# Optimization experiments

Hardware: AMD Instinct MI355X
Metric: run time of the kernel (lower is better)

Reference implementation:

```python
import jax, jax.numpy as jnp
import numpy as np

B, IN, H, E, N_EP, V_DIM = 4096, 1024, 16, 256, 2048, 64


def setup_inputs() -> dict:
    key = jax.random.key(0)
    k_x, k_c, k_w, k_k, k_v = jax.random.split(key, 5)
    x = jax.random.normal(k_x, (B, IN), dtype=jnp.float32)
    curiosity_score = jax.random.normal(k_c, (B,), dtype=jnp.float32)
    # toqueries: Linear(IN, E*H, bias=False); store as [IN, E*H] for x @ Wq
    Wq = jax.random.normal(k_w, (IN, E * H), dtype=jnp.float32) * (1.0 / np.sqrt(IN))
    # offline_keys [n_episodes, emb_size]; buffer repeats over heads (identical), so keep 2D
    keys = jax.random.normal(k_k, (N_EP, E), dtype=jnp.float32)
    # values buffer = offline_values.abs().mean(dim=-1) -> [n_episodes]
    offline_values = jax.random.normal(k_v, (N_EP, V_DIM), dtype=jnp.float32)
    values = jnp.abs(offline_values).mean(axis=-1)
    return {"x": x, "curiosity_score": curiosity_score, "Wq": Wq, "keys": keys, "values": values}


def reference(x, curiosity_score, Wq, keys, values):
    b = x.shape[0]
    # queries: [b, h, e], scaled by e**(1/4) (keys left unscaled, as in source)
    q = (x @ Wq).reshape(b, H, E) / (E ** 0.25)
    # dot: [b, h, n_episodes]; keys identical across heads -> single contraction
    dot = jnp.einsum("bhe,ne->bhn", q, keys) + values[None, None, :]
    dot = jax.nn.softmax(dot, axis=-1)
    # curiosity reweighting: scale probabilities then re-softmax (not scale-invariant)
    cur = jnp.exp(curiosity_score).reshape(b, 1, 1)
    dot = jax.nn.softmax(dot * cur, axis=-1)
    # head-mean -> [b, n_episodes]
    return dot.mean(axis=1)
```

## Files before the change

kernel.cpp:

```cpp
#include <hip/hip_runtime.h>


typedef __attribute__((ext_vector_type(8))) short bf16x8;
typedef __attribute__((ext_vector_type(4))) float f32x4;

typedef const __attribute__((address_space(1))) void* gcptr;
typedef __attribute__((address_space(3))) void* sptr;

__device__ __forceinline__ void gload16(const void* g, void* l) {
  __builtin_amdgcn_global_load_lds((gcptr)g, (sptr)l, 16, 0, 0);
}

__device__ __forceinline__ unsigned short f2bf(float f) {
  unsigned int u = __float_as_uint(f);
  unsigned int r = (u + 0x7fffu + ((u >> 16) & 1u)) >> 16;
  return (unsigned short)r;
}
__device__ __forceinline__ float bf2f(unsigned short s) {
  return __uint_as_float(((unsigned int)s) << 16);
}

__global__ void k_split(const float* __restrict__ src,
                        unsigned short* __restrict__ hi,
                        unsigned short* __restrict__ lo, int n4) {
  int i = blockIdx.x * blockDim.x + threadIdx.x;
  if (i >= n4) return;
  float4 v = reinterpret_cast<const float4*>(src)[i];
  ushort4 h, l;
  h.x = f2bf(v.x); l.x = f2bf(v.x - bf2f(h.x));
  h.y = f2bf(v.y); l.y = f2bf(v.y - bf2f(h.y));
  h.z = f2bf(v.z); l.z = f2bf(v.z - bf2f(h.z));
  h.w = f2bf(v.w); l.w = f2bf(v.w - bf2f(h.w));
  reinterpret_cast<ushort4*>(hi)[i] = h;
  reinterpret_cast<ushort4*>(lo)[i] = l;
}

__global__ void k_prepk(const float* __restrict__ keys,
                        unsigned short* __restrict__ th,
                        unsigned short* __restrict__ tl) {
  int g = blockIdx.x * blockDim.x + threadIdx.x;
  int k0 = g >> 13, rem = g & 8191;
  int jg = rem >> 6, lam = rem & 63;
  int row = jg * 16 + (lam & 15);
  int col = k0 * 32 + (lam >> 4) * 8;
  const float* s = keys + (size_t)row * 256 + col;
  float4 v0 = *reinterpret_cast<const float4*>(s);
  float4 v1 = *reinterpret_cast<const float4*>(s + 4);
  ushort4 h0, h1, l0, l1;
  h0.x = f2bf(v0.x); l0.x = f2bf(v0.x - bf2f(h0.x));
  h0.y = f2bf(v0.y); l0.y = f2bf(v0.y - bf2f(h0.y));
  h0.z = f2bf(v0.z); l0.z = f2bf(v0.z - bf2f(h0.z));
  h0.w = f2bf(v0.w); l0.w = f2bf(v0.w - bf2f(h0.w));
  h1.x = f2bf(v1.x); l1.x = f2bf(v1.x - bf2f(h1.x));
  h1.y = f2bf(v1.y); l1.y = f2bf(v1.y - bf2f(h1.y));
  h1.z = f2bf(v1.z); l1.z = f2bf(v1.z - bf2f(h1.z));
  h1.w = f2bf(v1.w); l1.w = f2bf(v1.w - bf2f(h1.w));
  reinterpret_cast<ushort4*>(th + (size_t)g * 8)[0] = h0;
  reinterpret_cast<ushort4*>(th + (size_t)g * 8)[1] = h1;
  reinterpret_cast<ushort4*>(tl + (size_t)g * 8)[0] = l0;
  reinterpret_cast<ushort4*>(tl + (size_t)g * 8)[1] = l1;
}

__global__ void k_twq(const float* __restrict__ W,
                      unsigned short* __restrict__ th,
                      unsigned short* __restrict__ tl) {
  __shared__ float t[64][65];
  int tx = threadIdx.x & 63, ty = threadIdx.x >> 6;
  int c0 = blockIdx.x * 64, r0 = blockIdx.y * 64;
#pragma unroll
  for (int i = 0; i < 64; i += 4)
    t[ty + i][tx] = W[(size_t)(r0 + ty + i) * 4096 + (c0 + tx)] * 0.25f;
  __syncthreads();
#pragma unroll
  for (int i = 0; i < 64; i += 4) {
    float v = t[tx][ty + i];
    unsigned short h = f2bf(v);
    unsigned short l = f2bf(v - bf2f(h));
    size_t o = (size_t)(c0 + ty + i) * 1024 + (r0 + tx);
    th[o] = h; tl[o] = l;
  }
}

__global__ __launch_bounds__(256) void k_gemm1(
    const unsigned short* __restrict__ Ah, const unsigned short* __restrict__ Al,
    const unsigned short* __restrict__ Bh, const unsigned short* __restrict__ Bl,
    unsigned short* __restrict__ Qh, unsigned short* __restrict__ Ql) {
  __shared__ unsigned short As[2][128][32];
  __shared__ unsigned short Bs[2][128][32];
  const int tid = threadIdx.x;
  const int w = tid >> 6, l = tid & 63;
  const int lr = l & 15, lg = l >> 4;
  const int m0 = blockIdx.y * 128, n0 = blockIdx.x * 128;
  const int wr = (w >> 1) * 64, wc = (w & 1) * 64;
  const int srow = tid >> 2;
  const int skel = (tid & 3) * 8;
  f32x4 acc[4][4] = {};

  const size_t gaBase = (size_t)(m0 + srow) * 1024 + skel;
  const size_t gbBase = (size_t)(n0 + srow) * 1024 + skel;
  char* lA0 = (char*)&As[0][0][0] + w * 1024;
  char* lA1 = (char*)&As[1][0][0] + w * 1024;
  char* lB0 = (char*)&Bs[0][0][0] + w * 1024;
  char* lB1 = (char*)&Bs[1][0][0] + w * 1024;

  for (int k0 = 0; k0 < 1024; k0 += 32) {
    gload16(Ah + gaBase + k0,             lA0);
    gload16(Ah + gaBase + 64 * 1024 + k0, lA0 + 4096);
    gload16(Al + gaBase + k0,             lA1);
    gload16(Al + gaBase + 64 * 1024 + k0, lA1 + 4096);
    gload16(Bh + gbBase + k0,             lB0);
    gload16(Bh + gbBase + 64 * 1024 + k0, lB0 + 4096);
    gload16(Bl + gbBase + k0,             lB1);
    gload16(Bl + gbBase + 64 * 1024 + k0, lB1 + 4096);
    __syncthreads();
    bf16x8 ah[4], am[4], bh[4], bm[4];
#pragma unroll
    for (int i = 0; i < 4; ++i) {
      ah[i] = *reinterpret_cast<const bf16x8*>(&As[0][wr + i * 16 + lr][lg * 8]);
      am[i] = *reinterpret_cast<const bf16x8*>(&As[1][wr + i * 16 + lr][lg * 8]);
      bh[i] = *reinterpret_cast<const bf16x8*>(&Bs[0][wc + i * 16 + lr][lg * 8]);
      bm[i] = *reinterpret_cast<const bf16x8*>(&Bs[1][wc + i * 16 + lr][lg * 8]);
    }
#pragma unroll
    for (int i = 0; i < 4; ++i)
#pragma unroll
      for (int j = 0; j < 4; ++j) {
        acc[i][j] = __builtin_amdgcn_mfma_f32_16x16x32_bf16(ah[i], bh[j], acc[i][j], 0, 0, 0);
        acc[i][j] = __builtin_amdgcn_mfma_f32_16x16x32_bf16(am[i], bh[j], acc[i][j], 0, 0, 0);
        acc[i][j] = __builtin_amdgcn_mfma_f32_16x16x32_bf16(ah[i], bm[j], acc[i][j], 0, 0, 0);
      }
    __syncthreads();
  }
#pragma unroll
  for (int i = 0; i < 4; ++i)
#pragma unroll
    for (int j = 0; j < 4; ++j)
#pragma unroll
      for (int r = 0; r < 4; ++r) {
        int row = m0 + wr + i * 16 + lg * 4 + r;
        int col = n0 + wc + j * 16 + lr;
        float v = acc[i][j][r];
        unsigned short hh = f2bf(v);
        unsigned short ll = f2bf(v - bf2f(hh));
        size_t o = (size_t)row * 4096 + col;
        Qh[o] = hh; Ql[o] = ll;
      }
}

#define MFMA_BF16(a, b, c) __builtin_amdgcn_mfma_f32_16x16x32_bf16(a, b, c, 0, 0, 0)

#define C_OF(T) ((unsigned)((((T) >> 4) * 128 + ((T) & 15)) * 1024))

#define LOADB(SLOT, T)                                                        \
  B##SLOT = *reinterpret_cast<const bf16x8*>(kHb + (vbase + C_OF(T)));        \
  L##SLOT = *reinterpret_cast<const bf16x8*>(kLb + (vbase + C_OF(T)));

#define DJST(J0, J1, S0, S1, PF, T0, T1)              \
  __builtin_amdgcn_s_setprio(1);                      \
  acc[0][J0] = MFMA_BF16(ah0, B##S0, acc[0][J0]);     \
  acc[1][J0] = MFMA_BF16(ah1, B##S0, acc[1][J0]);     \
  acc[0][J1] = MFMA_BF16(ah0, B##S1, acc[0][J1]);     \
  acc[1][J1] = MFMA_BF16(ah1, B##S1, acc[1][J1]);     \
  acc[0][J0] = MFMA_BF16(am0, B##S0, acc[0][J0]);     \
  acc[1][J0] = MFMA_BF16(am1, B##S0, acc[1][J0]);     \
  acc[0][J1] = MFMA_BF16(am0, B##S1, acc[0][J1]);     \
  acc[1][J1] = MFMA_BF16(am1, B##S1, acc[1][J1]);     \
  acc[0][J0] = MFMA_BF16(ah0, L##S0, acc[0][J0]);     \
  acc[1][J0] = MFMA_BF16(ah1, L##S0, acc[1][J0]);     \
  acc[0][J1] = MFMA_BF16(ah0, L##S1, acc[0][J1]);     \
  acc[1][J1] = MFMA_BF16(ah1, L##S1, acc[1][J1]);     \
  __builtin_amdgcn_s_setprio(0);                      \
  if (PF) { LOADB(S0, T0) LOADB(S1, T1) }

#define BODY_HEAD(K)                                                   \
  ah0 = *reinterpret_cast<const bf16x8*>(As + ((K)) * 512 + l8);       \
  ah1 = *reinterpret_cast<const bf16x8*>(As + (8 + (K)) * 512 + l8);   \
  am0 = *reinterpret_cast<const bf16x8*>(As + (16 + (K)) * 512 + l8);  \
  am1 = *reinterpret_cast<const bf16x8*>(As + (24 + (K)) * 512 + l8);

#define BODY(K)                                            \
  BODY_HEAD(K)                                             \
  DJST(0,  1,  0, 1, 1, (K) * 16 + 4,  (K) * 16 + 5)       \
  DJST(2,  3,  2, 3, 1, (K) * 16 + 6,  (K) * 16 + 7)       \
  DJST(4,  5,  0, 1, 1, (K) * 16 + 8,  (K) * 16 + 9)       \
  DJST(6,  7,  2, 3, 1, (K) * 16 + 10, (K) * 16 + 11)      \
  DJST(8,  9,  0, 1, 1, (K) * 16 + 12, (K) * 16 + 13)      \
  DJST(10, 11, 2, 3, 1, (K) * 16 + 14, (K) * 16 + 15)      \
  DJST(12, 13, 0, 1, 1, (K) * 16 + 16, (K) * 16 + 17)      \
  DJST(14, 15, 2, 3, 1, (K) * 16 + 18, (K) * 16 + 19)

#define BODY7                              \
  BODY_HEAD(7)                             \
  DJST(0,  1,  0, 1, 1, 116, 117)          \
  DJST(2,  3,  2, 3, 1, 118, 119)          \
  DJST(4,  5,  0, 1, 1, 120, 121)          \
  DJST(6,  7,  2, 3, 1, 122, 123)          \
  DJST(8,  9,  0, 1, 1, 124, 125)          \
  DJST(10, 11, 2, 3, 1, 126, 127)          \
  DJST(12, 13, 0, 1, 0, 0, 0)              \
  DJST(14, 15, 2, 3, 0, 0, 0)

__global__ __launch_bounds__(512, 2) void k_attn(
    const unsigned short* __restrict__ Qh, const unsigned short* __restrict__ Ql,
    const unsigned short* __restrict__ KtH, const unsigned short* __restrict__ KtL,
    const float* __restrict__ values, const float* __restrict__ cur,
    float* __restrict__ out) {
  __shared__ unsigned short As[32 * 512];
  __shared__ float red[8][32];
  const int tid = threadIdx.x;
  const int w = tid >> 6, l = tid & 63;
  const int lr = l & 15, lg = l >> 4;
  const int r0 = blockIdx.x * 32;
  const int cs = (int)((w + blockIdx.x) & 7);
  const int n0 = cs * 256;
  const int l8 = l * 8;

#pragma unroll
  for (int qq = 0; qq < 4; ++qq) {
    const int s = w * 4 + qq;
    const int plane = s >> 4, mf = (s >> 3) & 1, k0s = s & 7;
    const unsigned short* src = plane ? Ql : Qh;
    const size_t ga = (size_t)(r0 + mf * 16 + lr) * 256 + k0s * 32 + lg * 8;
    gload16(src + ga, (char*)As + s * 1024);
  }
  __syncthreads();

  const unsigned sliceB = (unsigned)__builtin_amdgcn_readfirstlane(cs * 16384);
  const char* kHb = (const char*)KtH + sliceB;
  const char* kLb = (const char*)KtL + sliceB;
  const unsigned vbase = (unsigned)(l * 16);

  f32x4 acc[2][16] = {};
  bf16x8 B0, B1, B2, B3, L0, L1, L2, L3;
  bf16x8 ah0, ah1, am0, am1;

  LOADB(0, 0) LOADB(1, 1) LOADB(2, 2) LOADB(3, 3)

  BODY(0) BODY(1) BODY(2) BODY(3) BODY(4) BODY(5) BODY(6) BODY7

#pragma unroll
  for (int j = 0; j < 16; ++j) {
    float vv = values[n0 + j * 16 + lr];
#pragma unroll
    for (int mf = 0; mf < 2; ++mf)
#pragma unroll
      for (int r = 0; r < 4; ++r) acc[mf][j][r] += vv;
  }

  const int rb = lg * 4;
  float M1[2][4];
#pragma unroll
  for (int mf = 0; mf < 2; ++mf)
#pragma unroll
    for (int r = 0; r < 4; ++r) {
      float m = acc[mf][0][r];
#pragma unroll
      for (int j = 1; j < 16; ++j) m = fmaxf(m, acc[mf][j][r]);
      m = fmaxf(m, __shfl_xor(m, 1));
      m = fmaxf(m, __shfl_xor(m, 2));
      m = fmaxf(m, __shfl_xor(m, 4));
      m = fmaxf(m, __shfl_xor(m, 8));
      M1[mf][r] = m;
    }
  if (lr == 0) {
#pragma unroll
    for (int mf = 0; mf < 2; ++mf)
#pragma unroll
      for (int r = 0; r < 4; ++r) red[w][mf * 16 + rb + r] = M1[mf][r];
  }
  __syncthreads();
#pragma unroll
  for (int mf = 0; mf < 2; ++mf)
#pragma unroll
    for (int r = 0; r < 4; ++r) {
      float m = red[0][mf * 16 + rb + r];
#pragma unroll
      for (int w2 = 1; w2 < 8; ++w2) m = fmaxf(m, red[w2][mf * 16 + rb + r]);
      M1[mf][r] = m;
    }
  __syncthreads();
  float Z1[2][4];
#pragma unroll
  for (int mf = 0; mf < 2; ++mf)
#pragma unroll
    for (int r = 0; r < 4; ++r) {
      float z = 0.f;
#pragma unroll
      for (int j = 0; j < 16; ++j) {
        float e = __expf(acc[mf][j][r] - M1[mf][r]);
        acc[mf][j][r] = e;
        z += e;
      }
      z += __shfl_xor(z, 1); z += __shfl_xor(z, 2);
      z += __shfl_xor(z, 4); z += __shfl_xor(z, 8);
      Z1[mf][r] = z;
    }
  if (lr == 0) {
#pragma unroll
    for (int mf = 0; mf < 2; ++mf)
#pragma unroll
      for (int r = 0; r < 4; ++r) red[w][mf * 16 + rb + r] = Z1[mf][r];
  }
  __syncthreads();
#pragma unroll
  for (int mf = 0; mf < 2; ++mf)
#pragma unroll
    for (int r = 0; r < 4; ++r) {
      float z = 0.f;
#pragma unroll
      for (int w2 = 0; w2 < 8; ++w2) z += red[w2][mf * 16 + rb + r];
      Z1[mf][r] = z;
    }
  __syncthreads();
  const float c0 = __expf(cur[(r0 >> 4) + 0]);
  const float c1 = __expf(cur[(r0 >> 4) + 1]);
  float Z2[2][4];
#pragma unroll
  for (int mf = 0; mf < 2; ++mf)
#pragma unroll
    for (int r = 0; r < 4; ++r) {
      float s2 = (mf ? c1 : c0) / Z1[mf][r];
      float z = 0.f;
#pragma unroll
      for (int j = 0; j < 16; ++j) {
        float o = __expf(s2 * (acc[mf][j][r] - 1.0f));
        acc[mf][j][r] = o;
        z += o;
      }
      z += __shfl_xor(z, 1); z += __shfl_xor(z, 2);
      z += __shfl_xor(z, 4); z += __shfl_xor(z, 8);
      Z2[mf][r] = z;
    }
  if (lr == 0) {
#pragma unroll
    for (int mf = 0; mf < 2; ++mf)
#pragma unroll
      for (int r = 0; r < 4; ++r) red[w][mf * 16 + rb + r] = Z2[mf][r];
  }
  __syncthreads();
#pragma unroll
  for (int mf = 0; mf < 2; ++mf)
#pragma unroll
    for (int r = 0; r < 4; ++r) {
      float z = 0.f;
#pragma unroll
      for (int w2 = 0; w2 < 8; ++w2) z += red[w2][mf * 16 + rb + r];
      Z2[mf][r] = z;
    }
  float rz[2][4];
#pragma unroll
  for (int mf = 0; mf < 2; ++mf)
#pragma unroll
    for (int r = 0; r < 4; ++r) rz[mf][r] = 1.0f / (16.0f * Z2[mf][r]);
#pragma unroll
  for (int mf = 0; mf < 2; ++mf)
#pragma unroll
    for (int j = 0; j < 16; ++j) {
      float s = acc[mf][j][0] * rz[mf][0] + acc[mf][j][1] * rz[mf][1] +
                acc[mf][j][2] * rz[mf][2] + acc[mf][j][3] * rz[mf][3];
      s += __shfl_xor(s, 16);
      s += __shfl_xor(s, 32);
      if (l < 16)
        out[(size_t)((r0 >> 4) + mf) * 2048 + n0 + j * 16 + l] = s;
    }
}

extern "C" void kernel_launch(void* const* d_in, const int* in_sizes, int n_in,
                              void* d_out, int out_size, void* d_ws, size_t ws_size,
                              hipStream_t stream) {
  const float* x    = (const float*)d_in[0];
  const float* cur  = (const float*)d_in[1];
  const float* Wq   = (const float*)d_in[2];
  const float* keys = (const float*)d_in[3];
  const float* vals = (const float*)d_in[4];
  float* out = (float*)d_out;

  char* ws = (char*)d_ws;
  unsigned short* x_hi = (unsigned short*)ws;  ws += (size_t)4096 * 1024 * 2;
  unsigned short* x_lo = (unsigned short*)ws;  ws += (size_t)4096 * 1024 * 2;
  unsigned short* w_hi = (unsigned short*)ws;  ws += (size_t)4096 * 1024 * 2;
  unsigned short* w_lo = (unsigned short*)ws;  ws += (size_t)4096 * 1024 * 2;
  unsigned short* k_hi = (unsigned short*)ws;  ws += (size_t)2048 * 256 * 2;
  unsigned short* k_lo = (unsigned short*)ws;  ws += (size_t)2048 * 256 * 2;
  unsigned short* q_hi = (unsigned short*)ws;  ws += (size_t)4096 * 4096 * 2;
  unsigned short* q_lo = (unsigned short*)ws;

  k_split<<<4096, 256, 0, stream>>>(x, x_hi, x_lo, 4096 * 1024 / 4);
  k_prepk<<<256, 256, 0, stream>>>(keys, k_hi, k_lo);
  k_twq<<<dim3(64, 16), 256, 0, stream>>>(Wq, w_hi, w_lo);
  k_gemm1<<<dim3(32, 32), 256, 0, stream>>>(x_hi, x_lo, w_hi, w_lo, q_hi, q_lo);
  k_attn<<<2048, 512, 0, stream>>>(q_hi, q_lo, k_hi, k_lo, vals, cur, out);
}
```

Baseline: 378.3 us.

## Deepen key prefetch pipeline with LDS ring buffer for low-plane keys

Restructures the attention GEMM inner loop to prefetch eight key tiles ahead instead of four. The high-plane keys stay in registers, while the low-plane keys are loaded asynchronously into a per-wave LDS ring via global_load_lds and read back one step ahead. Explicit vmcnt waits gate each step. The aim is to hide global load latency behind the MFMAs without extra VGPR pressure, at the cost of 64KB more LDS per block, which may cut occupancy at two blocks per CU, plus the added LDS read traffic.

```diff
diff --git a/kernel.cpp b/kernel.cpp
--- a/kernel.cpp
+++ b/kernel.cpp
@@ -148,29 +148,25 @@
 }
 
 #define MFMA_BF16(a, b, c) __builtin_amdgcn_mfma_f32_16x16x32_bf16(a, b, c, 0, 0, 0)
-
-#define C_OF(T) ((unsigned)((((T) >> 4) * 128 + ((T) & 15)) * 1024))
-
-#define LOADB(SLOT, T)                                                        \
-  B##SLOT = *reinterpret_cast<const bf16x8*>(kHb + (vbase + C_OF(T)));        \
-  L##SLOT = *reinterpret_cast<const bf16x8*>(kLb + (vbase + C_OF(T)));
-
-#define DJST(J0, J1, S0, S1, PF, T0, T1)              \
-  __builtin_amdgcn_s_setprio(1);                      \
-  acc[0][J0] = MFMA_BF16(ah0, B##S0, acc[0][J0]);     \
-  acc[1][J0] = MFMA_BF16(ah1, B##S0, acc[1][J0]);     \
-  acc[0][J1] = MFMA_BF16(ah0, B##S1, acc[0][J1]);     \
-  acc[1][J1] = MFMA_BF16(ah1, B##S1, acc[1][J1]);     \
-  acc[0][J0] = MFMA_BF16(am0, B##S0, acc[0][J0]);     \
-  acc[1][J0] = MFMA_BF16(am1, B##S0, acc[1][J0]);     \
-  acc[0][J1] = MFMA_BF16(am0, B##S1, acc[0][J1]);     \
-  acc[1][J1] = MFMA_BF16(am1, B##S1, acc[1][J1]);     \
-  acc[0][J0] = MFMA_BF16(ah0, L##S0, acc[0][J0]);     \
-  acc[1][J0] = MFMA_BF16(ah1, L##S0, acc[1][J0]);     \
-  acc[0][J1] = MFMA_BF16(ah0, L##S1, acc[0][J1]);     \
-  acc[1][J1] = MFMA_BF16(ah1, L##S1, acc[1][J1]);     \
-  __builtin_amdgcn_s_setprio(0);                      \
-  if (PF) { LOADB(S0, T0) LOADB(S1, T1) }
+#define GATE(N) asm volatile("s_waitcnt vmcnt(" #N ")" ::: "memory")
+
+#define C_OF(T) ((unsigned)((((T) >> 4) * 131072) + (((T) & 15) * 1024)))
+
+#define JST(J, SLOT, NSLOT, CUR, NXT, GN, PF, TISS)                            \
+  GATE(GN);                                                                    \
+  NXT = *reinterpret_cast<const bf16x8*>(ringS + (NSLOT) * 512 + l8);          \
+  __builtin_amdgcn_s_setprio(1);                                               \
+  acc[0][J] = MFMA_BF16(ah0, B##SLOT, acc[0][J]);                              \
+  acc[1][J] = MFMA_BF16(ah1, B##SLOT, acc[1][J]);                              \
+  acc[0][J] = MFMA_BF16(am0, B##SLOT, acc[0][J]);                              \
+  acc[1][J] = MFMA_BF16(am1, B##SLOT, acc[1][J]);                              \
+  acc[0][J] = MFMA_BF16(ah0, CUR, acc[0][J]);                                  \
+  acc[1][J] = MFMA_BF16(ah1, CUR, acc[1][J]);                                  \
+  __builtin_amdgcn_s_setprio(0);                                               \
+  if (PF) {                                                                    \
+    B##SLOT = *reinterpret_cast<const bf16x8*>(kHb + (vbase + C_OF(TISS)));    \
+    gload16(kLb + (vbase + C_OF(TISS)), ringC + (SLOT) * 1024);                \
+  }
 
 #define BODY_HEAD(K)                                                   \
   ah0 = *reinterpret_cast<const bf16x8*>(As + ((K)) * 512 + l8);       \
@@ -178,35 +174,56 @@
   am0 = *reinterpret_cast<const bf16x8*>(As + (16 + (K)) * 512 + l8);  \
   am1 = *reinterpret_cast<const bf16x8*>(As + (24 + (K)) * 512 + l8);
 
-#define BODY(K)                                            \
-  BODY_HEAD(K)                                             \
-  DJST(0,  1,  0, 1, 1, (K) * 16 + 4,  (K) * 16 + 5)       \
-  DJST(2,  3,  2, 3, 1, (K) * 16 + 6,  (K) * 16 + 7)       \
-  DJST(4,  5,  0, 1, 1, (K) * 16 + 8,  (K) * 16 + 9)       \
-  DJST(6,  7,  2, 3, 1, (K) * 16 + 10, (K) * 16 + 11)      \
-  DJST(8,  9,  0, 1, 1, (K) * 16 + 12, (K) * 16 + 13)      \
-  DJST(10, 11, 2, 3, 1, (K) * 16 + 14, (K) * 16 + 15)      \
-  DJST(12, 13, 0, 1, 1, (K) * 16 + 16, (K) * 16 + 17)      \
-  DJST(14, 15, 2, 3, 1, (K) * 16 + 18, (K) * 16 + 19)
-
-#define BODY7                              \
-  BODY_HEAD(7)                             \
-  DJST(0,  1,  0, 1, 1, 116, 117)          \
-  DJST(2,  3,  2, 3, 1, 118, 119)          \
-  DJST(4,  5,  0, 1, 1, 120, 121)          \
-  DJST(6,  7,  2, 3, 1, 122, 123)          \
-  DJST(8,  9,  0, 1, 1, 124, 125)          \
-  DJST(10, 11, 2, 3, 1, 126, 127)          \
-  DJST(12, 13, 0, 1, 0, 0, 0)              \
-  DJST(14, 15, 2, 3, 0, 0, 0)
+#define BODY(K)                                      \
+  BODY_HEAD(K)                                       \
+  JST(0,  0, 1, LA, LB, 12, 1, (K) * 16 + 8)         \
+  JST(1,  1, 2, LB, LA, 12, 1, (K) * 16 + 9)         \
+  JST(2,  2, 3, LA, LB, 12, 1, (K) * 16 + 10)        \
+  JST(3,  3, 4, LB, LA, 12, 1, (K) * 16 + 11)        \
+  JST(4,  4, 5, LA, LB, 12, 1, (K) * 16 + 12)        \
+  JST(5,  5, 6, LB, LA, 12, 1, (K) * 16 + 13)        \
+  JST(6,  6, 7, LA, LB, 12, 1, (K) * 16 + 14)        \
+  JST(7,  7, 0, LB, LA, 12, 1, (K) * 16 + 15)        \
+  JST(8,  0, 1, LA, LB, 12, 1, (K) * 16 + 16)        \
+  JST(9,  1, 2, LB, LA, 12, 1, (K) * 16 + 17)        \
+  JST(10, 2, 3, LA, LB, 12, 1, (K) * 16 + 18)        \
+  JST(11, 3, 4, LB, LA, 12, 1, (K) * 16 + 19)        \
+  JST(12, 4, 5, LA, LB, 12, 1, (K) * 16 + 20)        \
+  JST(13, 5, 6, LB, LA, 12, 1, (K) * 16 + 21)        \
+  JST(14, 6, 7, LA, LB, 12, 1, (K) * 16 + 22)        \
+  JST(15, 7, 0, LB, LA, 12, 1, (K) * 16 + 23)
+
+#define BODY7                                \
+  BODY_HEAD(7)                               \
+  JST(0,  0, 1, LA, LB, 12, 1, 120)          \
+  JST(1,  1, 2, LB, LA, 12, 1, 121)          \
+  JST(2,  2, 3, LA, LB, 12, 1, 122)          \
+  JST(3,  3, 4, LB, LA, 12, 1, 123)          \
+  JST(4,  4, 5, LA, LB, 12, 1, 124)          \
+  JST(5,  5, 6, LB, LA, 12, 1, 125)          \
+  JST(6,  6, 7, LA, LB, 12, 1, 126)          \
+  JST(7,  7, 0, LB, LA, 12, 1, 127)          \
+  JST(8,  0, 1, LA, LB, 12, 0, 0)            \
+  JST(9,  1, 2, LB, LA, 10, 0, 0)            \
+  JST(10, 2, 3, LA, LB, 8,  0, 0)            \
+  JST(11, 3, 4, LB, LA, 6,  0, 0)            \
+  JST(12, 4, 5, LA, LB, 4,  0, 0)            \
+  JST(13, 5, 6, LB, LA, 2,  0, 0)            \
+  JST(14, 6, 7, LA, LB, 0,  0, 0)            \
+  JST(15, 7, 0, LB, LA, 0,  0, 0)
+
+#define LOADP(P)                                                         \
+  B##P = *reinterpret_cast<const bf16x8*>(kHb + (vbase + C_OF(P)));      \
+  gload16(kLb + (vbase + C_OF(P)), ringC + (P) * 1024);
 
 __global__ __launch_bounds__(512, 2) void k_attn(
     const unsigned short* __restrict__ Qh, const unsigned short* __restrict__ Ql,
     const unsigned short* __restrict__ KtH, const unsigned short* __restrict__ KtL,
     const float* __restrict__ values, const float* __restrict__ cur,
     float* __restrict__ out) {
-  __shared__ unsigned short As[32 * 512];
+  __shared__ unsigned short SM[49152];
   __shared__ float red[8][32];
+  unsigned short* As = SM;
   const int tid = threadIdx.x;
   const int w = tid >> 6, l = tid & 63;
   const int lr = l & 15, lg = l >> 4;
@@ -229,12 +246,17 @@
   const char* kHb = (const char*)KtH + sliceB;
   const char* kLb = (const char*)KtL + sliceB;
   const unsigned vbase = (unsigned)(l * 16);
+  unsigned short* ringS = SM + 16384 + w * 4096;
+  char* ringC = (char*)(SM + 16384) + w * 8192;
 
   f32x4 acc[2][16] = {};
-  bf16x8 B0, B1, B2, B3, L0, L1, L2, L3;
+  bf16x8 B0, B1, B2, B3, B4, B5, B6, B7;
+  bf16x8 LA, LB;
   bf16x8 ah0, ah1, am0, am1;
 
-  LOADB(0, 0) LOADB(1, 1) LOADB(2, 2) LOADB(3, 3)
+  LOADP(0) LOADP(1) LOADP(2) LOADP(3) LOADP(4) LOADP(5) LOADP(6) LOADP(7)
+  GATE(14);
+  LA = *reinterpret_cast<const bf16x8*>(ringS + l8);
 
   BODY(0) BODY(1) BODY(2) BODY(3) BODY(4) BODY(5) BODY(6) BODY7
 
```

Result: no change. 384.3 us (+1.6%).
